# Kernel tuning notes

Measured on AMD Instinct MI355X. Metric: run time of the kernel, lower is better.

The kernel has to match this reference:

```python
import jax, jax.numpy as jnp
import numpy as np

T = 2048          # num tokens (prefill)
H = 4096          # hidden_size
NH = 32           # num query heads
NKV = 8           # num kv heads (GQA)
HD = H // NH      # head_dim = 128
BASE = 1000000.0  # rope_theta
NEG = -1e30


def _rope(x, positions):
    # NeoX-style rotary embedding (vLLM default). x: [T, nh, HD]
    half = HD // 2
    inv_freq = 1.0 / (BASE ** (jnp.arange(half, dtype=jnp.float32) / half))
    freqs = positions.astype(jnp.float32)[:, None] * inv_freq  # [T, half]
    cos = jnp.concatenate([jnp.cos(freqs), jnp.cos(freqs)], -1)[:, None, :]
    sin = jnp.concatenate([jnp.sin(freqs), jnp.sin(freqs)], -1)[:, None, :]
    rot = jnp.concatenate([-x[..., half:], x[..., :half]], -1)
    return x * cos + rot * sin


def setup_inputs() -> dict:
    key = jax.random.key(0)
    k1, k2, k3 = jax.random.split(key, 3)
    hidden_states = jax.random.normal(k1, (T, H), jnp.float32)
    wqkv = jax.random.normal(k2, (H, (NH + 2 * NKV) * HD), jnp.float32) * 0.02
    wo = jax.random.normal(k3, (NH * HD, H), jnp.float32) * 0.02
    positions = jnp.arange(T, dtype=jnp.int32)
    return {"positions": positions, "hidden_states": hidden_states,
            "wqkv": wqkv, "wo": wo}


def reference(positions, hidden_states, wqkv, wo):
    # fused QKV projection
    qkv = hidden_states @ wqkv                      # [T, (NH+2*NKV)*HD]
    q, k, v = jnp.split(qkv, [NH * HD, NH * HD + NKV * HD], axis=-1)
    q = q.reshape(T, NH, HD)
    k = k.reshape(T, NKV, HD)
    v = v.reshape(T, NKV, HD)
    # inline RoPE on q, k
    q = _rope(q, positions)
    k = _rope(k, positions)
    # GQA: expand kv heads to query heads
    rep = NH // NKV
    k = jnp.repeat(k, rep, axis=1)                  # [T, NH, HD]
    v = jnp.repeat(v, rep, axis=1)
    # causal scaled dot-product attention (prefill path of PagedAttention)
    scores = jnp.einsum('qhd,khd->hqk', q, k) * (HD ** -0.5)  # [NH, T, T]
    causal = positions[:, None] >= positions[None, :]          # [T, T]
    scores = jnp.where(causal[None, :, :], scores, NEG)
    probs = jax.nn.softmax(scores, axis=-1)
    attn = jnp.einsum('hqk,khd->qhd', probs, v).reshape(T, NH * HD)
    return attn @ wo
```

## Files before the change

### kernel.cpp

```cpp
#include <hip/hip_runtime.h>
#include <hip/hip_bf16.h>

typedef __attribute__((ext_vector_type(8))) short bf16x8;
typedef __attribute__((ext_vector_type(4))) float f32x4;
typedef unsigned short u16;

#define T_TOK 2048
#define HID 4096
#define NH 32
#define NKV 8
#define HD 128
#define QKVN 6144
#define KOFF 4096
#define VOFF 5120
#define ATTN_SCALE 0.08838834764831845f

static __device__ __forceinline__ float bf2f(u16 x) {
    union { float f; unsigned u; } v; v.u = ((unsigned)x) << 16; return v.f;
}
static __device__ __forceinline__ u16 f2bf(float f) {
    union { float f; unsigned u; } v; v.f = f;
    unsigned u = v.u;
    unsigned r = (u + 0x7fff + ((u >> 16) & 1)) >> 16;
    return (u16)r;
}

static __device__ __forceinline__ void gload16(const u16* g, u16* l) {
    __builtin_amdgcn_global_load_lds((const __attribute__((address_space(1))) void*)g,
                                     (__attribute__((address_space(3))) void*)l, 16, 0, 0);
}

#define VMC(n) asm volatile("s_waitcnt vmcnt(%0)" :: "i"(n) : "memory")
#define LGKM0() asm volatile("s_waitcnt lgkmcnt(0)" ::: "memory")
#define BAR() __builtin_amdgcn_s_barrier()
#define SCHB() __builtin_amdgcn_sched_barrier(0)

__global__ __launch_bounds__(256) void convk(const float* __restrict__ in, u16* __restrict__ out) {
    int i = blockIdx.x * 256 + threadIdx.x;
    float4 v = ((const float4*)in)[i];
    ushort4 o;
    o.x = f2bf(v.x); o.y = f2bf(v.y); o.z = f2bf(v.z); o.w = f2bf(v.w);
    ((ushort4*)out)[i] = o;
}

__global__ __launch_bounds__(256) void transpk(const float* __restrict__ in, u16* __restrict__ out,
                                               int R, int C) {
    __shared__ float tile[64][65];
    int c0 = blockIdx.x * 64, r0 = blockIdx.y * 64;
    int tid = threadIdx.x;
#pragma unroll
    for (int it = 0; it < 4; ++it) {
        int ci = it * 256 + tid;
        int r = ci >> 4, c4 = (ci & 15) * 4;
        float4 v = *(const float4*)&in[(size_t)(r0 + r) * C + c0 + c4];
        tile[r][c4 + 0] = v.x; tile[r][c4 + 1] = v.y; tile[r][c4 + 2] = v.z; tile[r][c4 + 3] = v.w;
    }
    __syncthreads();
#pragma unroll
    for (int it = 0; it < 4; ++it) {
        int ci = it * 256 + tid;
        int c = ci >> 4, rq = (ci & 15) * 4;
        ushort4 o;
        o.x = f2bf(tile[rq + 0][c]); o.y = f2bf(tile[rq + 1][c]);
        o.z = f2bf(tile[rq + 2][c]); o.w = f2bf(tile[rq + 3][c]);
        *(ushort4*)&out[(size_t)(c0 + c) * R + r0 + rq] = o;
    }
}

__global__ __launch_bounds__(512, 2) void gemm256(const u16* __restrict__ A, const u16* __restrict__ Bt,
                                                  u16* __restrict__ Cout, int M, int N, int K) {
    constexpr int DBUF = 512 * 64;
    __shared__ __attribute__((aligned(16))) u16 lds[2 * DBUF];

    int bid = blockIdx.x;
    int m0 = (bid & 7) * 256, n0 = (bid >> 3) * 256;
    int tid = threadIdx.x, lane = tid & 63, wid = tid >> 6;
    int wm = wid >> 2, wn = wid & 3;
    int l15 = lane & 15, g4 = lane >> 4;
    int sw = l15 & 7;
    int srow8 = tid >> 3;
    int sslot8 = ((tid & 7) ^ (srow8 & 7)) * 8;
    int NK = K / 64;

    auto STAGE = [&](int kt, int c) {
        u16* dst = &lds[(kt & 1) * DBUF + c * 4096 + wid * 512];
        const u16* src = (c < 4)
            ? &A[(size_t)(m0 + c * 64 + srow8) * K + kt * 64 + sslot8]
            : &Bt[(size_t)(n0 + (c - 4) * 64 + srow8) * K + kt * 64 + sslot8];
        gload16(src, dst);
    };

    f32x4 acc[8][4];
#pragma unroll
    for (int i = 0; i < 8; ++i)
#pragma unroll
        for (int j = 0; j < 4; ++j) acc[i][j] = (f32x4){0.f, 0.f, 0.f, 0.f};

#pragma unroll
    for (int c = 0; c < 8; ++c) STAGE(0, c);
    VMC(0);
    BAR(); SCHB();

    for (int g = 0; g < NK; ++g) {
        const u16* ab = &lds[(g & 1) * DBUF];
        const u16* bb = ab + 16384;
        bool st = (g + 1 < NK);
        bf16x8 af[8], af2[8], b0, b1;

#pragma unroll
        for (int mi = 0; mi < 8; ++mi)
            af[mi] = *(const bf16x8*)&ab[(wm * 128 + mi * 16 + l15) * 64 + ((g4 ^ sw) * 8)];
        b0 = *(const bf16x8*)&bb[(wn * 64 + 0 * 16 + l15) * 64 + ((g4 ^ sw) * 8)];
        b1 = *(const bf16x8*)&bb[(wn * 64 + 1 * 16 + l15) * 64 + ((g4 ^ sw) * 8)];
        if (st) { STAGE(g + 1, 0); STAGE(g + 1, 1); STAGE(g + 1, 4); }
        BAR(); LGKM0();
        __builtin_amdgcn_s_setprio(1);
#pragma unroll
        for (int mi = 0; mi < 8; ++mi) {
            acc[mi][0] = __builtin_amdgcn_mfma_f32_16x16x32_bf16(af[mi], b0, acc[mi][0], 0, 0, 0);
            acc[mi][1] = __builtin_amdgcn_mfma_f32_16x16x32_bf16(af[mi], b1, acc[mi][1], 0, 0, 0);
        }
        __builtin_amdgcn_s_setprio(0);
        BAR();

        b0 = *(const bf16x8*)&bb[(wn * 64 + 2 * 16 + l15) * 64 + ((g4 ^ sw) * 8)];
        b1 = *(const bf16x8*)&bb[(wn * 64 + 3 * 16 + l15) * 64 + ((g4 ^ sw) * 8)];
#pragma unroll
        for (int mi = 0; mi < 4; ++mi)
            af2[mi] = *(const bf16x8*)&ab[(wm * 128 + mi * 16 + l15) * 64 + (((4 + g4) ^ sw) * 8)];
        if (st) { STAGE(g + 1, 2); STAGE(g + 1, 3); STAGE(g + 1, 5); }
        BAR(); LGKM0();
        __builtin_amdgcn_s_setprio(1);
#pragma unroll
        for (int mi = 0; mi < 8; ++mi) {
            acc[mi][2] = __builtin_amdgcn_mfma_f32_16x16x32_bf16(af[mi], b0, acc[mi][2], 0, 0, 0);
            acc[mi][3] = __builtin_amdgcn_mfma_f32_16x16x32_bf16(af[mi], b1, acc[mi][3], 0, 0, 0);
        }
        __builtin_amdgcn_s_setprio(0);
        BAR();

#pragma unroll
        for (int mi = 4; mi < 8; ++mi)
            af2[mi] = *(const bf16x8*)&ab[(wm * 128 + mi * 16 + l15) * 64 + (((4 + g4) ^ sw) * 8)];
        b0 = *(const bf16x8*)&bb[(wn * 64 + 0 * 16 + l15) * 64 + (((4 + g4) ^ sw) * 8)];
        b1 = *(const bf16x8*)&bb[(wn * 64 + 1 * 16 + l15) * 64 + (((4 + g4) ^ sw) * 8)];
        if (st) { STAGE(g + 1, 6); STAGE(g + 1, 7); }
        BAR(); LGKM0();
        __builtin_amdgcn_s_setprio(1);
#pragma unroll
        for (int mi = 0; mi < 8; ++mi) {
            acc[mi][0] = __builtin_amdgcn_mfma_f32_16x16x32_bf16(af2[mi], b0, acc[mi][0], 0, 0, 0);
            acc[mi][1] = __builtin_amdgcn_mfma_f32_16x16x32_bf16(af2[mi], b1, acc[mi][1], 0, 0, 0);
        }
        __builtin_amdgcn_s_setprio(0);
        BAR();

        b0 = *(const bf16x8*)&bb[(wn * 64 + 2 * 16 + l15) * 64 + (((4 + g4) ^ sw) * 8)];
        b1 = *(const bf16x8*)&bb[(wn * 64 + 3 * 16 + l15) * 64 + (((4 + g4) ^ sw) * 8)];
        BAR(); LGKM0();
        __builtin_amdgcn_s_setprio(1);
#pragma unroll
        for (int mi = 0; mi < 8; ++mi) {
            acc[mi][2] = __builtin_amdgcn_mfma_f32_16x16x32_bf16(af2[mi], b0, acc[mi][2], 0, 0, 0);
            acc[mi][3] = __builtin_amdgcn_mfma_f32_16x16x32_bf16(af2[mi], b1, acc[mi][3], 0, 0, 0);
        }
        __builtin_amdgcn_s_setprio(0);
        if (st) VMC(0);
        BAR(); SCHB();
    }

#pragma unroll
    for (int mi = 0; mi < 8; ++mi)
#pragma unroll
        for (int nj = 0; nj < 4; ++nj)
#pragma unroll
            for (int i = 0; i < 4; ++i) {
                int row = m0 + wm * 128 + mi * 16 + g4 * 4 + i;
                int col = n0 + wn * 64 + nj * 16 + l15;
                Cout[(size_t)row * N + col] = f2bf(acc[mi][nj][i]);
            }
}

template <int BN, int OUTF32>
__global__ __launch_bounds__(512) void gemm4p(const u16* __restrict__ A, const u16* __restrict__ Bt,
                                              void* __restrict__ Cout, int M, int N, int K) {
    constexpr int NF = BN / 64;
    constexpr int LB = BN / 128;
    constexpr int DBUF = (128 + BN) * 64;
    constexpr int BHALF = (BN / 2) * 64;
    __shared__ __attribute__((aligned(16))) u16 lds[2 * DBUF];

    int bid = blockIdx.x;
    int m0 = (bid & 15) * 128, n0 = (bid >> 4) * BN;
    int tid = threadIdx.x, lane = tid & 63, wid = tid >> 6;
    int wm = wid >> 2, wn = wid & 3;
    int l15 = lane & 15, g4 = lane >> 4;
    int sw = l15 & 7;
    int srow = tid >> 3;
    int sslot8 = (((tid & 7) ^ ((tid >> 3) & 7))) * 8;
    int brow0 = (wn & 1) * (BN / 4);
    int NK = K / 64;

    auto STAGE_A = [&](int kt, int h) {
        gload16(&A[(size_t)(m0 + h * 64 + srow) * K + kt * 64 + sslot8],
                &lds[(kt & 1) * DBUF + h * 4096 + wid * 512]);
    };
    auto STAGE_B = [&](int kt, int bh) {
#pragma unroll
        for (int it = 0; it < LB; ++it)
            gload16(&Bt[(size_t)(n0 + bh * (BN / 2) + it * 64 + srow) * K + kt * 64 + sslot8],
                    &lds[(kt & 1) * DBUF + 8192 + bh * BHALF + it * 4096 + wid * 512]);
    };

    f32x4 acc[4][NF];
#pragma unroll
    for (int i = 0; i < 4; ++i)
#pragma unroll
        for (int j = 0; j < NF; ++j) acc[i][j] = (f32x4){0.f, 0.f, 0.f, 0.f};

    STAGE_A(0, 0); STAGE_A(0, 1); STAGE_B(0, 0); STAGE_B(0, 1);
    STAGE_A(1, 0); STAGE_A(1, 1); STAGE_B(1, 0); STAGE_B(1, 1);
    VMC(2 + 2 * LB);
    BAR(); SCHB();

    for (int g = 0; g < NK; ++g) {
        const u16* dd = &lds[(g & 1) * DBUF];
        const u16* aw = dd + wm * 4096;
        const u16* bw = dd + 8192 + (wn >> 1) * BHALF;
        bool mid = (g > 0) && (g + 1 < NK);
        bf16x8 bfr[NF], af0, af1;

#pragma unroll
        for (int nf = 0; nf < NF; ++nf)
            bfr[nf] = *(const bf16x8*)&bw[(brow0 + nf * 16 + l15) * 64 + ((g4 ^ sw) * 8)];
        af0 = *(const bf16x8*)&aw[(0 * 16 + l15) * 64 + ((g4 ^ sw) * 8)];
        af1 = *(const bf16x8*)&aw[(1 * 16 + l15) * 64 + ((g4 ^ sw) * 8)];
        if (mid) STAGE_A(g + 1, 0);
        BAR(); LGKM0();
        __builtin_amdgcn_s_setprio(1);
#pragma unroll
        for (int nf = 0; nf < NF; ++nf) {
            acc[0][nf] = __builtin_amdgcn_mfma_f32_16x16x32_bf16(af0, bfr[nf], acc[0][nf], 0, 0, 0);
            acc[1][nf] = __builtin_amdgcn_mfma_f32_16x16x32_bf16(af1, bfr[nf], acc[1][nf], 0, 0, 0);
        }
        __builtin_amdgcn_s_setprio(0);
        BAR();

        af0 = *(const bf16x8*)&aw[(2 * 16 + l15) * 64 + ((g4 ^ sw) * 8)];
        af1 = *(const bf16x8*)&aw[(3 * 16 + l15) * 64 + ((g4 ^ sw) * 8)];
        if (mid) STAGE_B(g + 1, 1);
        BAR(); LGKM0();
        __builtin_amdgcn_s_setprio(1);
#pragma unroll
        for (int nf = 0; nf < NF; ++nf) {
            acc[2][nf] = __builtin_amdgcn_mfma_f32_16x16x32_bf16(af0, bfr[nf], acc[2][nf], 0, 0, 0);
            acc[3][nf] = __builtin_amdgcn_mfma_f32_16x16x32_bf16(af1, bfr[nf], acc[3][nf], 0, 0, 0);
        }
        __builtin_amdgcn_s_setprio(0);
        BAR();

#pragma unroll
        for (int nf = 0; nf < NF; ++nf)
            bfr[nf] = *(const bf16x8*)&bw[(brow0 + nf * 16 + l15) * 64 + (((4 + g4) ^ sw) * 8)];
        af0 = *(const bf16x8*)&aw[(0 * 16 + l15) * 64 + (((4 + g4) ^ sw) * 8)];
        af1 = *(const bf16x8*)&aw[(1 * 16 + l15) * 64 + (((4 + g4) ^ sw) * 8)];
        if (mid) STAGE_A(g + 1, 1);
        BAR(); LGKM0();
        __builtin_amdgcn_s_setprio(1);
#pragma unroll
        for (int nf = 0; nf < NF; ++nf) {
            acc[0][nf] = __builtin_amdgcn_mfma_f32_16x16x32_bf16(af0, bfr[nf], acc[0][nf], 0, 0, 0);
            acc[1][nf] = __builtin_amdgcn_mfma_f32_16x16x32_bf16(af1, bfr[nf], acc[1][nf], 0, 0, 0);
        }
        __builtin_amdgcn_s_setprio(0);
        BAR();

        af0 = *(const bf16x8*)&aw[(2 * 16 + l15) * 64 + (((4 + g4) ^ sw) * 8)];
        af1 = *(const bf16x8*)&aw[(3 * 16 + l15) * 64 + (((4 + g4) ^ sw) * 8)];
        if (g + 2 < NK) STAGE_B(g + 2, 0);
        BAR(); LGKM0();
        __builtin_amdgcn_s_setprio(1);
#pragma unroll
        for (int nf = 0; nf < NF; ++nf) {
            acc[2][nf] = __builtin_amdgcn_mfma_f32_16x16x32_bf16(af0, bfr[nf], acc[2][nf], 0, 0, 0);
            acc[3][nf] = __builtin_amdgcn_mfma_f32_16x16x32_bf16(af1, bfr[nf], acc[3][nf], 0, 0, 0);
        }
        __builtin_amdgcn_s_setprio(0);
        if (g <= NK - 3)      VMC(LB);
        else if (g == NK - 2) VMC(0);
        BAR(); SCHB();
    }

#pragma unroll
    for (int mf = 0; mf < 4; ++mf)
#pragma unroll
        for (int nf = 0; nf < NF; ++nf)
#pragma unroll
            for (int i = 0; i < 4; ++i) {
                int row = m0 + wm * 64 + mf * 16 + g4 * 4 + i;
                int col = n0 + wn * (BN / 4) + nf * 16 + l15;
                float v = acc[mf][nf][i];
                if (OUTF32) ((float*)Cout)[(size_t)row * N + col] = v;
                else        ((u16*)Cout)[(size_t)row * N + col] = f2bf(v);
            }
}

__global__ __launch_bounds__(256) void ropek(u16* __restrict__ qkvb, const int* __restrict__ positions) {
    __shared__ float cs_[64], sn_[64];
    int t = blockIdx.x;
    float pos = (float)positions[t];
    if (threadIdx.x < 64) {
        int d = threadIdx.x;
        float inv = exp2f(-(float)d * (19.931568569324174f / 64.0f));
        float fr = pos * inv;
        cs_[d] = cosf(fr);
        sn_[d] = sinf(fr);
    }
    __syncthreads();
#pragma unroll
    for (int it = 0; it < 10; ++it) {
        int ci = it * 256 + threadIdx.x;
        int hh = ci >> 6, d = ci & 63;
        int base = (hh < NH) ? hh * HD : KOFF + (hh - NH) * HD;
        size_t off = (size_t)t * QKVN + base + d;
        float x1 = bf2f(qkvb[off]);
        float x2 = bf2f(qkvb[off + 64]);
        float s = sn_[d], c = cs_[d];
        float y1 = x1 * c - x2 * s;
        float y2 = x2 * c + x1 * s;
        if (hh < NH) { y1 *= ATTN_SCALE; y2 *= ATTN_SCALE; }
        qkvb[off]      = f2bf(y1);
        qkvb[off + 64] = f2bf(y2);
    }
}

__global__ __launch_bounds__(256) void vtranspk(const u16* __restrict__ qkvb, u16* __restrict__ vT) {
    __shared__ __attribute__((aligned(16))) u16 tile[64][136];
    int kvh = blockIdx.x, t0 = blockIdx.y * 64;
    int tid = threadIdx.x;
#pragma unroll
    for (int it = 0; it < 4; ++it) {
        int ci = it * 256 + tid;
        int r = ci >> 4, c8 = (ci & 15) * 8;
        *(bf16x8*)&tile[r][c8] = *(const bf16x8*)&qkvb[(size_t)(t0 + r) * QKVN + VOFF + kvh * HD + c8];
    }
    __syncthreads();
#pragma unroll
    for (int it = 0; it < 4; ++it) {
        int ci = it * 256 + tid;
        int d = ci >> 3, tc = (ci & 7) * 8;
        union { bf16x8 v; u16 u[8]; } o;
#pragma unroll
        for (int e = 0; e < 8; ++e) o.u[e] = tile[tc + e][d];
        *(bf16x8*)&vT[((size_t)kvh * HD + d) * T_TOK + t0 + tc] = o.v;
    }
}

__global__ __launch_bounds__(512) void attnk(const u16* __restrict__ qkvb, const u16* __restrict__ vT,
                                             u16* __restrict__ attnb) {
    __shared__ __attribute__((aligned(16))) u16 kt_[64 * 132];
    __shared__ __attribute__((aligned(16))) u16 vt_[128 * 68];
    __shared__ __attribute__((aligned(16))) u16 pl_[8 * 16 * 68];
    int h = blockIdx.x, qt = 15 - blockIdx.y;
    int kvh = h >> 2;
    int q0 = qt * 128;
    int tid = threadIdx.x, lane = tid & 63, wid = tid >> 6;
    int l15 = lane & 15, g = lane >> 4;

    const u16* kbase = qkvb + KOFF + (size_t)kvh * HD;
    const u16* vbase = vT + (size_t)kvh * HD * T_TOK;

    bf16x8 qf[4];
    int qrow = q0 + wid * 16 + l15;
#pragma unroll
    for (int ks = 0; ks < 4; ++ks)
        qf[ks] = *(const bf16x8*)&qkvb[(size_t)qrow * QKVN + h * HD + ks * 32 + g * 8];

    f32x4 o[8];
#pragma unroll
    for (int df = 0; df < 8; ++df) o[df] = (f32x4){0.f, 0.f, 0.f, 0.f};
    float m_run[4], l_run[4];
#pragma unroll
    for (int i = 0; i < 4; ++i) { m_run[i] = -3.0e38f; l_run[i] = 0.f; }

    int NT = 2 * qt + 2;

    bf16x8 kreg[2], vreg[2];
#pragma unroll
    for (int it = 0; it < 2; ++it) {
        int gi = it * 512 + tid;
        kreg[it] = *(const bf16x8*)&kbase[(size_t)(gi >> 4) * QKVN + (gi & 15) * 8];
        vreg[it] = *(const bf16x8*)&vbase[(size_t)(gi >> 3) * T_TOK + (gi & 7) * 8];
    }
#pragma unroll
    for (int it = 0; it < 2; ++it) {
        int gi = it * 512 + tid;
        *(bf16x8*)&kt_[(gi >> 4) * 132 + (gi & 15) * 8] = kreg[it];
        *(bf16x8*)&vt_[(gi >> 3) * 68 + (gi & 7) * 8] = vreg[it];
    }
#pragma unroll
    for (int it = 0; it < 2; ++it) {
        int gi = it * 512 + tid;
        kreg[it] = *(const bf16x8*)&kbase[(size_t)(64 + (gi >> 4)) * QKVN + (gi & 15) * 8];
        vreg[it] = *(const bf16x8*)&vbase[(size_t)(gi >> 3) * T_TOK + 64 + (gi & 7) * 8];
    }
    __syncthreads();

    for (int kt2 = 0; kt2 < NT; ++kt2) {
        int kvb = kt2 * 64;
        bool active = (kvb <= q0 + wid * 16 + 15);
        bool diag   = (kvb + 63 > q0 + wid * 16);

        if (active) {
            f32x4 s[4];
#pragma unroll
            for (int nf = 0; nf < 4; ++nf) s[nf] = (f32x4){0.f, 0.f, 0.f, 0.f};
            __builtin_amdgcn_s_setprio(1);
#pragma unroll
            for (int ks = 0; ks < 4; ++ks) {
#pragma unroll
                for (int nf = 0; nf < 4; ++nf) {
                    bf16x8 bfr = *(const bf16x8*)&kt_[(nf * 16 + l15) * 132 + ks * 32 + g * 8];
                    s[nf] = __builtin_amdgcn_mfma_f32_16x16x32_bf16(qf[ks], bfr, s[nf], 0, 0, 0);
                }
            }
            __builtin_amdgcn_s_setprio(0);

            float mrow[4];
#pragma unroll
            for (int i = 0; i < 4; ++i) {
                int qr = q0 + wid * 16 + g * 4 + i;
                float mx = -3.0e38f;
#pragma unroll
                for (int nf = 0; nf < 4; ++nf) {
                    float v = s[nf][i];
                    if (diag) {
                        int kvc = kvb + nf * 16 + l15;
                        v = (kvc <= qr) ? v : -1.0e30f;
                        s[nf][i] = v;
                    }
                    mx = fmaxf(mx, v);
                }
                mrow[i] = mx;
            }
#pragma unroll
            for (int dd = 1; dd < 16; dd <<= 1)
#pragma unroll
                for (int i = 0; i < 4; ++i) mrow[i] = fmaxf(mrow[i], __shfl_xor(mrow[i], dd));

            int ok = 1;
#pragma unroll
            for (int i = 0; i < 4; ++i) ok &= (mrow[i] <= m_run[i] + 8.0f) ? 1 : 0;
            if (!__all(ok)) {
                float alpha[4];
#pragma unroll
                for (int i = 0; i < 4; ++i) {
                    float mnew = fmaxf(m_run[i], mrow[i]);
                    alpha[i] = __expf(m_run[i] - mnew);
                    m_run[i] = mnew;
                    l_run[i] *= alpha[i];
                }
#pragma unroll
                for (int df = 0; df < 8; ++df)
#pragma unroll
                    for (int i = 0; i < 4; ++i) o[df][i] *= alpha[i];
            }

            float rsum[4] = {0.f, 0.f, 0.f, 0.f};
#pragma unroll
            for (int nf = 0; nf < 4; ++nf)
#pragma unroll
                for (int i = 0; i < 4; ++i) {
                    float p = __expf(s[nf][i] - m_run[i]);
                    rsum[i] += p;
                    pl_[wid * 1088 + (g * 4 + i) * 68 + nf * 16 + l15] = f2bf(p);
                }
#pragma unroll
            for (int dd = 1; dd < 16; dd <<= 1)
#pragma unroll
                for (int i = 0; i < 4; ++i) rsum[i] += __shfl_xor(rsum[i], dd);
#pragma unroll
            for (int i = 0; i < 4; ++i) l_run[i] += rsum[i];

            __builtin_amdgcn_s_setprio(1);
#pragma unroll
            for (int ks2 = 0; ks2 < 2; ++ks2) {
                bf16x8 af = *(const bf16x8*)&pl_[wid * 1088 + l15 * 68 + ks2 * 32 + g * 8];
#pragma unroll
                for (int df = 0; df < 8; ++df) {
                    bf16x8 bfr = *(const bf16x8*)&vt_[(df * 16 + l15) * 68 + ks2 * 32 + g * 8];
                    o[df] = __builtin_amdgcn_mfma_f32_16x16x32_bf16(af, bfr, o[df], 0, 0, 0);
                }
            }
            __builtin_amdgcn_s_setprio(0);
        }

        if (kt2 < NT - 1) {
            __syncthreads();
#pragma unroll
            for (int it = 0; it < 2; ++it) {
                int gi = it * 512 + tid;
                *(bf16x8*)&kt_[(gi >> 4) * 132 + (gi & 15) * 8] = kreg[it];
                *(bf16x8*)&vt_[(gi >> 3) * 68 + (gi & 7) * 8] = vreg[it];
            }
            int ktl = (kt2 + 2 < NT) ? kt2 + 2 : NT - 1;
#pragma unroll
            for (int it = 0; it < 2; ++it) {
                int gi = it * 512 + tid;
                kreg[it] = *(const bf16x8*)&kbase[(size_t)(ktl * 64 + (gi >> 4)) * QKVN + (gi & 15) * 8];
                vreg[it] = *(const bf16x8*)&vbase[(size_t)(gi >> 3) * T_TOK + ktl * 64 + (gi & 7) * 8];
            }
            __syncthreads();
        }
    }

#pragma unroll
    for (int df = 0; df < 8; ++df)
#pragma unroll
        for (int i = 0; i < 4; ++i) {
            int qr = q0 + wid * 16 + g * 4 + i;
            int col = h * HD + df * 16 + l15;
            attnb[(size_t)qr * (NH * HD) + col] = f2bf(o[df][i] / l_run[i]);
        }
}

extern "C" void kernel_launch(void* const* d_in, const int* in_sizes, int n_in,
                              void* d_out, int out_size, void* d_ws, size_t ws_size,
                              hipStream_t stream) {
    const int*   positions = (const int*)d_in[0];
    const float* hs        = (const float*)d_in[1];
    const float* wqkv      = (const float*)d_in[2];
    const float* wo        = (const float*)d_in[3];
    float* out = (float*)d_out;

    char* ws = (char*)d_ws;
    u16* hsb   = (u16*)(ws);
    u16* wqkvT = (u16*)(ws + 16777216);
    u16* woT   = (u16*)(ws + 16777216 + 50331648);
    u16* qkvb  = (u16*)(ws + 16777216 + 50331648 + 33554432);
    u16* vT    = (u16*)(ws + 16777216 + 50331648 + 33554432 + 25165824);
    u16* attnb = hsb;

    convk<<<8192, 256, 0, stream>>>(hs, hsb);
    transpk<<<dim3(96, 64), 256, 0, stream>>>(wqkv, wqkvT, HID, QKVN);
    transpk<<<dim3(64, 64), 256, 0, stream>>>(wo, woT, HID, HID);

    gemm256<<<dim3(192), 512, 0, stream>>>(hsb, wqkvT, qkvb, T_TOK, QKVN, HID);

    ropek<<<T_TOK, 256, 0, stream>>>(qkvb, positions);

    vtranspk<<<dim3(NKV, 32), 256, 0, stream>>>(qkvb, vT);

    attnk<<<dim3(NH, 16), 512, 0, stream>>>(qkvb, vT, attnb);

    gemm4p<256, 1><<<dim3(256), 512, 0, stream>>>(attnb, woT, out, T_TOK, HID, HID);
}
```

Measured before the change: 346.4 us.

## Restructure QKV GEMM pipeline, remap block tiles, and defer softmax row reductions

The 256x256 GEMM now uses 8 half-tile stages with a deeper prefetch: stages are issued two k-steps ahead and waited on with a partial vmcnt. Each wave's fragments are interleaved across tile halves, and the B fragments are kept in registers through four MFMA phases. Block-to-tile mapping in both GEMMs is remapped so concurrently running blocks share B columns, aiming for better L2 reuse. In attention, the cross-lane max reduction runs only when the rescale check fails, and the row-sum shuffle reduction is deferred to the epilogue. This removes per-tile shuffles, at the cost of a more complex schedule and a local-max check that is correct but more conservative.

Result: faster. 329.6 us (-4.8%).

```diff
diff --git a/kernel.cpp b/kernel.cpp
--- a/kernel.cpp
+++ b/kernel.cpp
@@ -67,27 +67,28 @@
     }
 }
 
-__global__ __launch_bounds__(512, 2) void gemm256(const u16* __restrict__ A, const u16* __restrict__ Bt,
-                                                  u16* __restrict__ Cout, int M, int N, int K) {
-    constexpr int DBUF = 512 * 64;
-    __shared__ __attribute__((aligned(16))) u16 lds[2 * DBUF];
-
+__global__ __launch_bounds__(512) void gemm256(const u16* __restrict__ A, const u16* __restrict__ Bt,
+                                               u16* __restrict__ Cout, int M, int N, int K) {
+    __shared__ __attribute__((aligned(16))) u16 lds[65536];
     int bid = blockIdx.x;
-    int m0 = (bid & 7) * 256, n0 = (bid >> 3) * 256;
+    int m0 = ((bid >> 3) & 7) * 256;
+    int n0 = ((bid & 7) * 3 + (bid >> 6)) * 256;
     int tid = threadIdx.x, lane = tid & 63, wid = tid >> 6;
     int wm = wid >> 2, wn = wid & 3;
     int l15 = lane & 15, g4 = lane >> 4;
     int sw = l15 & 7;
-    int srow8 = tid >> 3;
-    int sslot8 = ((tid & 7) ^ (srow8 & 7)) * 8;
     int NK = K / 64;
-
-    auto STAGE = [&](int kt, int c) {
-        u16* dst = &lds[(kt & 1) * DBUF + c * 4096 + wid * 512];
-        const u16* src = (c < 4)
-            ? &A[(size_t)(m0 + c * 64 + srow8) * K + kt * 64 + sslot8]
-            : &Bt[(size_t)(n0 + (c - 4) * 64 + srow8) * K + kt * 64 + sslot8];
-        gload16(src, dst);
+    int sslot8 = ((tid & 7) ^ ((tid >> 3) & 7)) * 8;
+
+    auto STAGE = [&](int kt, int half) {
+#pragma unroll
+        for (int c = 0; c < 2; ++c) {
+            int row = c * 64 + (tid >> 3);
+            const u16* src = (half < 2)
+                ? &A[(size_t)(m0 + half * 128 + row) * K + kt * 64 + sslot8]
+                : &Bt[(size_t)(n0 + (half - 2) * 128 + row) * K + kt * 64 + sslot8];
+            gload16(src, &lds[(kt & 1) * 32768 + half * 8192 + c * 4096 + tid * 8]);
+        }
     };
 
     f32x4 acc[8][4];
@@ -96,76 +97,93 @@
 #pragma unroll
         for (int j = 0; j < 4; ++j) acc[i][j] = (f32x4){0.f, 0.f, 0.f, 0.f};
 
-#pragma unroll
-    for (int c = 0; c < 8; ++c) STAGE(0, c);
-    VMC(0);
+    STAGE(0, 0); STAGE(0, 2); STAGE(0, 1); STAGE(0, 3); STAGE(1, 0); STAGE(1, 2);
+    VMC(4);
     BAR(); SCHB();
 
-    for (int g = 0; g < NK; ++g) {
-        const u16* ab = &lds[(g & 1) * DBUF];
-        const u16* bb = ab + 16384;
-        bool st = (g + 1 < NK);
-        bf16x8 af[8], af2[8], b0, b1;
-
-#pragma unroll
-        for (int mi = 0; mi < 8; ++mi)
-            af[mi] = *(const bf16x8*)&ab[(wm * 128 + mi * 16 + l15) * 64 + ((g4 ^ sw) * 8)];
-        b0 = *(const bf16x8*)&bb[(wn * 64 + 0 * 16 + l15) * 64 + ((g4 ^ sw) * 8)];
-        b1 = *(const bf16x8*)&bb[(wn * 64 + 1 * 16 + l15) * 64 + ((g4 ^ sw) * 8)];
-        if (st) { STAGE(g + 1, 0); STAGE(g + 1, 1); STAGE(g + 1, 4); }
-        BAR(); LGKM0();
-        __builtin_amdgcn_s_setprio(1);
-#pragma unroll
-        for (int mi = 0; mi < 8; ++mi) {
-            acc[mi][0] = __builtin_amdgcn_mfma_f32_16x16x32_bf16(af[mi], b0, acc[mi][0], 0, 0, 0);
-            acc[mi][1] = __builtin_amdgcn_mfma_f32_16x16x32_bf16(af[mi], b1, acc[mi][1], 0, 0, 0);
-        }
-        __builtin_amdgcn_s_setprio(0);
-        BAR();
-
-        b0 = *(const bf16x8*)&bb[(wn * 64 + 2 * 16 + l15) * 64 + ((g4 ^ sw) * 8)];
-        b1 = *(const bf16x8*)&bb[(wn * 64 + 3 * 16 + l15) * 64 + ((g4 ^ sw) * 8)];
+    for (int T = 0; T < NK; ++T) {
+        const u16* db = &lds[(T & 1) * 32768];
+        bf16x8 a[8], b0[4], b1[4];
+
 #pragma unroll
         for (int mi = 0; mi < 4; ++mi)
-            af2[mi] = *(const bf16x8*)&ab[(wm * 128 + mi * 16 + l15) * 64 + (((4 + g4) ^ sw) * 8)];
-        if (st) { STAGE(g + 1, 2); STAGE(g + 1, 3); STAGE(g + 1, 5); }
-        BAR(); LGKM0();
-        __builtin_amdgcn_s_setprio(1);
-#pragma unroll
-        for (int mi = 0; mi < 8; ++mi) {
-            acc[mi][2] = __builtin_amdgcn_mfma_f32_16x16x32_bf16(af[mi], b0, acc[mi][2], 0, 0, 0);
-            acc[mi][3] = __builtin_amdgcn_mfma_f32_16x16x32_bf16(af[mi], b1, acc[mi][3], 0, 0, 0);
-        }
-        __builtin_amdgcn_s_setprio(0);
-        BAR();
-
-#pragma unroll
-        for (int mi = 4; mi < 8; ++mi)
-            af2[mi] = *(const bf16x8*)&ab[(wm * 128 + mi * 16 + l15) * 64 + (((4 + g4) ^ sw) * 8)];
-        b0 = *(const bf16x8*)&bb[(wn * 64 + 0 * 16 + l15) * 64 + (((4 + g4) ^ sw) * 8)];
-        b1 = *(const bf16x8*)&bb[(wn * 64 + 1 * 16 + l15) * 64 + (((4 + g4) ^ sw) * 8)];
-        if (st) { STAGE(g + 1, 6); STAGE(g + 1, 7); }
-        BAR(); LGKM0();
-        __builtin_amdgcn_s_setprio(1);
-#pragma unroll
-        for (int mi = 0; mi < 8; ++mi) {
-            acc[mi][0] = __builtin_amdgcn_mfma_f32_16x16x32_bf16(af2[mi], b0, acc[mi][0], 0, 0, 0);
-            acc[mi][1] = __builtin_amdgcn_mfma_f32_16x16x32_bf16(af2[mi], b1, acc[mi][1], 0, 0, 0);
-        }
-        __builtin_amdgcn_s_setprio(0);
-        BAR();
-
-        b0 = *(const bf16x8*)&bb[(wn * 64 + 2 * 16 + l15) * 64 + (((4 + g4) ^ sw) * 8)];
-        b1 = *(const bf16x8*)&bb[(wn * 64 + 3 * 16 + l15) * 64 + (((4 + g4) ^ sw) * 8)];
-        BAR(); LGKM0();
-        __builtin_amdgcn_s_setprio(1);
-#pragma unroll
-        for (int mi = 0; mi < 8; ++mi) {
-            acc[mi][2] = __builtin_amdgcn_mfma_f32_16x16x32_bf16(af2[mi], b0, acc[mi][2], 0, 0, 0);
-            acc[mi][3] = __builtin_amdgcn_mfma_f32_16x16x32_bf16(af2[mi], b1, acc[mi][3], 0, 0, 0);
-        }
-        __builtin_amdgcn_s_setprio(0);
-        if (st) VMC(0);
+#pragma unroll
+            for (int ks = 0; ks < 2; ++ks) {
+                int r = mi * 32 + wm * 16 + l15;
+                a[mi * 2 + ks] = *(const bf16x8*)&db[0 * 8192 + r * 64 + (((ks << 2) + g4) ^ sw) * 8];
+            }
+#pragma unroll
+        for (int nj = 0; nj < 2; ++nj)
+#pragma unroll
+            for (int ks = 0; ks < 2; ++ks) {
+                int r = nj * 64 + wn * 16 + l15;
+                b0[nj * 2 + ks] = *(const bf16x8*)&db[2 * 8192 + r * 64 + (((ks << 2) + g4) ^ sw) * 8];
+            }
+        if (T + 1 < NK) STAGE(T + 1, 1);
+        BAR(); LGKM0(); SCHB();
+        __builtin_amdgcn_s_setprio(1);
+#pragma unroll
+        for (int mi = 0; mi < 4; ++mi)
+#pragma unroll
+            for (int nj = 0; nj < 2; ++nj)
+#pragma unroll
+                for (int ks = 0; ks < 2; ++ks)
+                    acc[mi][nj] = __builtin_amdgcn_mfma_f32_16x16x32_bf16(a[mi * 2 + ks], b0[nj * 2 + ks], acc[mi][nj], 0, 0, 0);
+        __builtin_amdgcn_s_setprio(0);
+        BAR();
+
+#pragma unroll
+        for (int nj = 0; nj < 2; ++nj)
+#pragma unroll
+            for (int ks = 0; ks < 2; ++ks) {
+                int r = nj * 64 + wn * 16 + l15;
+                b1[nj * 2 + ks] = *(const bf16x8*)&db[3 * 8192 + r * 64 + (((ks << 2) + g4) ^ sw) * 8];
+            }
+        if (T + 1 < NK) STAGE(T + 1, 3);
+        BAR(); LGKM0(); SCHB();
+        __builtin_amdgcn_s_setprio(1);
+#pragma unroll
+        for (int mi = 0; mi < 4; ++mi)
+#pragma unroll
+            for (int nj = 0; nj < 2; ++nj)
+#pragma unroll
+                for (int ks = 0; ks < 2; ++ks)
+                    acc[mi][2 + nj] = __builtin_amdgcn_mfma_f32_16x16x32_bf16(a[mi * 2 + ks], b1[nj * 2 + ks], acc[mi][2 + nj], 0, 0, 0);
+        __builtin_amdgcn_s_setprio(0);
+        BAR();
+
+#pragma unroll
+        for (int mi = 0; mi < 4; ++mi)
+#pragma unroll
+            for (int ks = 0; ks < 2; ++ks) {
+                int r = mi * 32 + wm * 16 + l15;
+                a[mi * 2 + ks] = *(const bf16x8*)&db[1 * 8192 + r * 64 + (((ks << 2) + g4) ^ sw) * 8];
+            }
+        if (T + 2 < NK) STAGE(T + 2, 0);
+        BAR(); LGKM0(); SCHB();
+        __builtin_amdgcn_s_setprio(1);
+#pragma unroll
+        for (int mi = 0; mi < 4; ++mi)
+#pragma unroll
+            for (int nj = 0; nj < 2; ++nj)
+#pragma unroll
+                for (int ks = 0; ks < 2; ++ks)
+                    acc[4 + mi][nj] = __builtin_amdgcn_mfma_f32_16x16x32_bf16(a[mi * 2 + ks], b0[nj * 2 + ks], acc[4 + mi][nj], 0, 0, 0);
+        __builtin_amdgcn_s_setprio(0);
+        BAR();
+
+        if (T + 2 < NK) STAGE(T + 2, 2);
+        BAR();
+        __builtin_amdgcn_s_setprio(1);
+#pragma unroll
+        for (int mi = 0; mi < 4; ++mi)
+#pragma unroll
+            for (int nj = 0; nj < 2; ++nj)
+#pragma unroll
+                for (int ks = 0; ks < 2; ++ks)
+                    acc[4 + mi][2 + nj] = __builtin_amdgcn_mfma_f32_16x16x32_bf16(a[mi * 2 + ks], b1[nj * 2 + ks], acc[4 + mi][2 + nj], 0, 0, 0);
+        __builtin_amdgcn_s_setprio(0);
+        if (T + 2 < NK) VMC(4); else VMC(0);
         BAR(); SCHB();
     }
 
@@ -175,8 +193,8 @@
         for (int nj = 0; nj < 4; ++nj)
 #pragma unroll
             for (int i = 0; i < 4; ++i) {
-                int row = m0 + wm * 128 + mi * 16 + g4 * 4 + i;
-                int col = n0 + wn * 64 + nj * 16 + l15;
+                int row = m0 + (mi >> 2) * 128 + (mi & 3) * 32 + wm * 16 + g4 * 4 + i;
+                int col = n0 + (nj >> 1) * 128 + (nj & 1) * 64 + wn * 16 + l15;
                 Cout[(size_t)row * N + col] = f2bf(acc[mi][nj][i]);
             }
 }
@@ -191,7 +209,8 @@
     __shared__ __attribute__((aligned(16))) u16 lds[2 * DBUF];
 
     int bid = blockIdx.x;
-    int m0 = (bid & 15) * 128, n0 = (bid >> 4) * BN;
+    int m0 = ((bid >> 3) & 15) * 128;
+    int n0 = ((bid & 7) * 2 + (bid >> 7)) * BN;
     int tid = threadIdx.x, lane = tid & 63, wid = tid >> 6;
     int wm = wid >> 2, wn = wid & 3;
     int l15 = lane & 15, g4 = lane >> 4;
@@ -426,7 +445,7 @@
             }
             __builtin_amdgcn_s_setprio(0);
 
-            float mrow[4];
+            float mloc[4];
 #pragma unroll
             for (int i = 0; i < 4; ++i) {
                 int qr = q0 + wid * 16 + g * 4 + i;
@@ -441,17 +460,20 @@
                     }
                     mx = fmaxf(mx, v);
                 }
-                mrow[i] = mx;
-            }
-#pragma unroll
-            for (int dd = 1; dd < 16; dd <<= 1)
-#pragma unroll
-                for (int i = 0; i < 4; ++i) mrow[i] = fmaxf(mrow[i], __shfl_xor(mrow[i], dd));
+                mloc[i] = mx;
+            }
 
             int ok = 1;
 #pragma unroll
-            for (int i = 0; i < 4; ++i) ok &= (mrow[i] <= m_run[i] + 8.0f) ? 1 : 0;
+            for (int i = 0; i < 4; ++i) ok &= (mloc[i] <= m_run[i] + 8.0f) ? 1 : 0;
             if (!__all(ok)) {
+                float mrow[4];
+#pragma unroll
+                for (int i = 0; i < 4; ++i) mrow[i] = mloc[i];
+#pragma unroll
+                for (int dd = 1; dd < 16; dd <<= 1)
+#pragma unroll
+                    for (int i = 0; i < 4; ++i) mrow[i] = fmaxf(mrow[i], __shfl_xor(mrow[i], dd));
                 float alpha[4];
 #pragma unroll
                 for (int i = 0; i < 4; ++i) {
@@ -466,21 +488,14 @@
                     for (int i = 0; i < 4; ++i) o[df][i] *= alpha[i];
             }
 
-            float rsum[4] = {0.f, 0.f, 0.f, 0.f};
 #pragma unroll
             for (int nf = 0; nf < 4; ++nf)
 #pragma unroll
                 for (int i = 0; i < 4; ++i) {
                     float p = __expf(s[nf][i] - m_run[i]);
-                    rsum[i] += p;
+                    l_run[i] += p;
                     pl_[wid * 1088 + (g * 4 + i) * 68 + nf * 16 + l15] = f2bf(p);
                 }
-#pragma unroll
-            for (int dd = 1; dd < 16; dd <<= 1)
-#pragma unroll
-                for (int i = 0; i < 4; ++i) rsum[i] += __shfl_xor(rsum[i], dd);
-#pragma unroll
-            for (int i = 0; i < 4; ++i) l_run[i] += rsum[i];
 
             __builtin_amdgcn_s_setprio(1);
 #pragma unroll
@@ -513,6 +528,11 @@
             __syncthreads();
         }
     }
+
+#pragma unroll
+    for (int dd = 1; dd < 16; dd <<= 1)
+#pragma unroll
+        for (int i = 0; i < 4; ++i) l_run[i] += __shfl_xor(l_run[i], dd);
 
 #pragma unroll
     for (int df = 0; df < 8; ++df)
```
